# Kernel tuning notes

Hardware: AMD Instinct MI355X
Metric: run time of the kernel (lower is better)

The kernel has to match this reference:

```python
import jax, jax.numpy as jnp
import numpy as np

H = 32          # total heads
K = 8           # active heads per token
D = 128         # head_dim = embed_dim // active_heads
E = 1024        # embed_dim
S = 1024        # seq_len
MAX_SEQ = 8192
BASE = 10000.0
SCALE = D ** -0.5
LB_W = 0.01
ENT_W = 0.01


def _rope(v, cos, sin):
    # v: (T, D); cos/sin: (T, D)
    v1, v2 = v[:, : D // 2], v[:, D // 2:]
    rot = jnp.concatenate([-v2, v1], axis=-1)
    return v * cos + rot * sin


def setup_inputs() -> dict:
    key = jax.random.key(0)
    ks = jax.random.split(key, 6)
    x = jax.random.normal(ks[0], (1, S, E), jnp.float32)
    Wq = jax.random.normal(ks[1], (E, H * D), jnp.float32) * 0.02
    Wk = jax.random.normal(ks[2], (E, H * D), jnp.float32) * 0.02
    Wv = jax.random.normal(ks[3], (E, H * D), jnp.float32) * 0.02
    Wr = jax.random.normal(ks[4], (E, H), jnp.float32) * 0.02
    Wo = jax.random.normal(ks[5], (K * D, E), jnp.float32) * 0.02
    head_counts = jnp.zeros((1, H), jnp.int32)
    return {"x": x, "Wq": Wq, "Wk": Wk, "Wv": Wv, "Wr": Wr, "Wo": Wo,
            "head_counts": head_counts}


def reference(x, Wq, Wk, Wv, Wr, Wo, head_counts):
    # ---- routing (eval mode: no gumbel noise) ----
    logits = x @ Wr                                   # (1, S, H)
    soft_probs = jax.nn.softmax(logits, axis=-1)
    top_logits, head_idx = jax.lax.top_k(logits, K)   # (1, S, K)
    head_w = jax.nn.softmax(top_logits, axis=-1)      # (1, S, K)

    # ---- aux loss ----
    primary = head_idx[..., 0]                        # (1, S)
    one_hot_p = jax.nn.one_hot(primary, H, dtype=jnp.float32)
    f = one_hot_p.mean(axis=1)                        # (1, H)
    p = soft_probs.mean(axis=1)                       # (1, H)
    balance = H * (f * p).sum(axis=-1).mean()
    entropy = -(soft_probs * jnp.log(soft_probs + 1e-8)).sum(axis=-1)
    entropy_loss = -entropy.mean()
    z_loss = (jax.nn.logsumexp(logits, axis=-1) ** 2).mean() * 0.01
    aux_loss = LB_W * balance + ENT_W * entropy_loss + z_loss

    # ---- projections + per-token gather of selected heads ----
    q_all = (x @ Wq).reshape(1, S, H, D)
    k_all = (x @ Wk).reshape(1, S, H, D)
    v_all = (x @ Wv).reshape(1, S, H, D)
    gidx = head_idx[..., None]                        # (1, S, K, 1)
    q = jnp.take_along_axis(q_all, gidx, axis=2)[0].reshape(S * K, D)
    k = jnp.take_along_axis(k_all, gidx, axis=2)[0].reshape(S * K, D)
    v = jnp.take_along_axis(v_all, gidx, axis=2)[0].reshape(S * K, D)

    heads_flat = head_idx[0].reshape(S * K)           # (T,)

    # rank of each dispatched token within its head (exclusive prefix count)
    oh = jax.nn.one_hot(heads_flat, H, dtype=jnp.int32)   # (T, H)
    excl = jnp.cumsum(oh, axis=0) - oh
    rank = jnp.take_along_axis(excl, heads_flat[:, None], axis=1)[:, 0]
    positions = rank + head_counts[0, heads_flat]
    positions = jnp.clip(positions, 0, MAX_SEQ - 1)

    # ---- per-head RoPE with per-head position counters ----
    inv_freq = 1.0 / (BASE ** (jnp.arange(0, D, 2, dtype=jnp.float32) / D))
    freqs = positions.astype(jnp.float32)[:, None] * inv_freq[None, :]
    emb = jnp.concatenate([freqs, freqs], axis=-1)    # (T, D)
    cos, sin = jnp.cos(emb), jnp.sin(emb)
    q = _rope(q, cos, sin)
    k = _rope(k, cos, sin)

    # ---- block-diagonal-causal attention (same head, earlier dispatch order) ----
    idx = jnp.arange(S * K)
    mask = (heads_flat[:, None] == heads_flat[None, :]) & (idx[None, :] <= idx[:, None])
    scores = (q @ k.T) * SCALE                        # (T, T)
    scores = jnp.where(mask, scores, jnp.float32(-1e30))
    attn = jax.nn.softmax(scores, axis=-1)
    out = attn @ v                                    # (T, D)

    # ---- combine with routing weights + output projection ----
    out = out.reshape(S, K, D) * head_w[0][..., None]
    out = out.reshape(S, K * D) @ Wo                  # (S, E)
    output = out[None]                                # (1, S, E)

    updated_counts = head_counts + oh.sum(axis=0)[None]
    return output, updated_counts, aux_loss
```

## Files before the change

### kernel.cpp

```cpp
#include <hip/hip_runtime.h>
#include <math.h>

#define S 1024
#define E 1024
#define H 32
#define KSEL 8
#define D 128
#define HD 4096
#define SK 8192
#define MAXL 1024
#define CAP 9216
#define ATTN_SCALE 0.08838834764831845f
#define SSTR 36
#define PSTR 40

#define NROUTER 256
#define NCONV 832

typedef _Float16 half8 __attribute__((ext_vector_type(8)));
typedef _Float16 half4 __attribute__((ext_vector_type(4)));
typedef float floatx4 __attribute__((ext_vector_type(4)));
typedef float floatx16 __attribute__((ext_vector_type(16)));
typedef float f4 __attribute__((ext_vector_type(4)));

#define GLOAD_LDS16(gsrc, ldst) \
    __builtin_amdgcn_global_load_lds( \
        (const __attribute__((address_space(1))) void*)(gsrc), \
        (__attribute__((address_space(3))) void*)(ldst), 16, 0, 0)

__global__ __launch_bounds__(256) void router_conv_kernel(
    const float* __restrict__ x, const float* __restrict__ Wr,
    int* __restrict__ head_idx, float* __restrict__ head_w,
    float* __restrict__ pbuf, float* __restrict__ entz,
    _Float16* __restrict__ xh,
    const float* __restrict__ Wq, const float* __restrict__ Wk,
    const float* __restrict__ Wv, const float* __restrict__ Wo,
    _Float16* __restrict__ Wqkt, _Float16* __restrict__ Wot)
{
    int bid = blockIdx.x, tid = threadIdx.x;
    if (bid >= NROUTER) {
        __shared__ _Float16 tl[128 * 128];
        int cb = bid - NROUTER;
        int z, rem;
        if (cb < 768) { z = cb >> 8; rem = cb & 255; }
        else          { z = 3;       rem = cb - 768; }
        const float* W = (z == 0) ? Wq : (z == 1) ? Wk : (z == 2) ? Wv : Wo;
        _Float16* T = (z < 3) ? (Wqkt + (size_t)z * HD * E) : Wot;
        int C = (z < 3) ? HD : 1024;
        int nc = C >> 7;
        int c0 = (rem % nc) * 128;
        int r0 = (rem / nc) * 128;
        #pragma unroll
        for (int p = 0; p < 16; ++p) {
            int idx = p * 256 + tid;
            int rr = idx >> 5, cg = (idx & 31) * 4;
            f4 v = *(const f4*)&W[(size_t)(r0 + rr) * C + c0 + cg];
            half4 o;
            o.x = (_Float16)v.x; o.y = (_Float16)v.y;
            o.z = (_Float16)v.z; o.w = (_Float16)v.w;
            int sc = cg ^ (((rr >> 3) & 7) << 2);
            *(half4*)&tl[rr * 128 + sc] = o;
        }
        __syncthreads();
        #pragma unroll
        for (int p = 0; p < 8; ++p) {
            int chunk = p * 256 + tid;
            int cc = chunk >> 4, ch = chunk & 15;
            int cidx = cc ^ ((ch & 7) << 2);
            half8 o;
            #pragma unroll
            for (int j = 0; j < 8; ++j)
                o[j] = tl[(ch * 8 + j) * 128 + cidx];
            *(half8*)&T[(size_t)(c0 + cc) * 1024 + r0 + ch * 8] = o;
        }
        return;
    }
    int s = bid * 4 + (tid >> 6);
    int lane = tid & 63;
    int h = lane & 31, half = lane >> 5;
    const float* xr = x + (size_t)s * E + half * 512;
    const float* wr = Wr + (size_t)(half * 512) * H + h;
    float a0 = 0.f, a1 = 0.f, a2 = 0.f, a3 = 0.f;
    #pragma unroll 4
    for (int e = 0; e < 512; e += 4) {
        a0 += xr[e]     * wr[e * H];
        a1 += xr[e + 1] * wr[(e + 1) * H];
        a2 += xr[e + 2] * wr[(e + 2) * H];
        a3 += xr[e + 3] * wr[(e + 3) * H];
    }
    float acc = (a0 + a1) + (a2 + a3);
    acc += __shfl_xor(acc, 32, 64);
    float logit = acc;
    float m = logit;
    #pragma unroll
    for (int off = 16; off; off >>= 1) m = fmaxf(m, __shfl_xor(m, off, 64));
    float ex = expf(logit - m);
    float Z = ex;
    #pragma unroll
    for (int off = 16; off; off >>= 1) Z += __shfl_xor(Z, off, 64);
    float p = ex / Z;
    float es = p * logf(p + 1e-8f);
    #pragma unroll
    for (int off = 16; off; off >>= 1) es += __shfl_xor(es, off, 64);
    float lse = m + logf(Z);
    float lv = logit;
    float tv[KSEL]; int ti[KSEL];
    #pragma unroll
    for (int j = 0; j < KSEL; ++j) {
        float bv = lv; int bi = h;
        #pragma unroll
        for (int off = 16; off; off >>= 1) {
            float ov = __shfl_xor(bv, off, 64);
            int oi = __shfl_xor(bi, off, 64);
            if (ov > bv || (ov == bv && oi < bi)) { bv = ov; bi = oi; }
        }
        tv[j] = bv; ti[j] = bi;
        if (h == bi) lv = -INFINITY;
    }
    float Z2 = 0.f;
    #pragma unroll
    for (int j = 0; j < KSEL; ++j) Z2 += expf(tv[j] - tv[0]);
    if (lane < 32) pbuf[s * 32 + lane] = p;
    if (lane == 0) {
        entz[s * 2]     = es;
        entz[s * 2 + 1] = lse * lse;
        #pragma unroll
        for (int j = 0; j < KSEL; ++j) {
            head_idx[s * KSEL + j] = ti[j];
            head_w[s * KSEL + j]   = expf(tv[j] - tv[0]) / Z2;
        }
    }
    const float* xrow = x + (size_t)s * E;
    _Float16* xhrow = xh + (size_t)s * E;
    #pragma unroll
    for (int t = 0; t < 4; ++t) {
        int e = t * 256 + lane * 4;
        f4 v = *(const f4*)&xrow[e];
        half4 o;
        o.x = (_Float16)v.x; o.y = (_Float16)v.y; o.z = (_Float16)v.z; o.w = (_Float16)v.w;
        *(half4*)&xhrow[e] = o;
    }
}

__global__ __launch_bounds__(256) void scan_aux_kernel(
    const int* __restrict__ head_idx, const int* __restrict__ head_counts,
    int* __restrict__ order, int* __restrict__ hlen, float* __restrict__ out_counts,
    const float* __restrict__ pbuf, const float* __restrict__ entz,
    float* __restrict__ out_aux)
{
    int bid = blockIdx.x, tid = threadIdx.x;
    if (bid == H) {
        int hh = tid & 31, grp = tid >> 5;
        __shared__ float red[256], red2[256];
        __shared__ float psum[32];
        __shared__ int hist[32];
        if (tid < 32) hist[tid] = 0;
        float ps = 0.f;
        for (int s = grp; s < S; s += 8) ps += pbuf[s * 32 + hh];
        red[tid] = ps;
        float es = 0.f, zs = 0.f;
        for (int s = tid; s < S; s += 256) { es += entz[s * 2]; zs += entz[s * 2 + 1]; }
        red2[tid] = es;
        __syncthreads();
        if (grp == 0) {
            float v = 0.f;
            #pragma unroll
            for (int j = 0; j < 8; ++j) v += red[j * 32 + hh];
            psum[hh] = v;
        }
        __syncthreads();
        red[tid] = zs;
        for (int s = tid; s < S; s += 256)
            atomicAdd(&hist[head_idx[s * KSEL]], 1);
        __syncthreads();
        for (int stp = 128; stp; stp >>= 1) {
            if (tid < stp) { red[tid] += red[tid + stp]; red2[tid] += red2[tid + stp]; }
            __syncthreads();
        }
        if (tid == 0) {
            float bal = 0.f;
            for (int j = 0; j < H; ++j)
                bal += ((float)hist[j] / (float)S) * (psum[j] / (float)S);
            bal *= (float)H;
            float ent_loss = red2[0] / (float)S;
            float z = red[0] / (float)S * 0.01f;
            out_aux[0] = 0.01f * bal + 0.01f * ent_loss + z;
        }
        return;
    }
    int h = bid;
    int wave = tid >> 6, lane = tid & 63;
    __shared__ int wtot[4][4];
    int base = 0;
    int hc = head_counts[h];
    int v0 = head_idx[tid],       v1 = head_idx[256 + tid];
    int v2 = head_idx[512 + tid], v3 = head_idx[768 + tid];
    unsigned long long lt = (1ull << lane) - 1ull;
    for (int c0 = 0; c0 < SK; c0 += 1024) {
        int n0 = 0, n1 = 0, n2 = 0, n3 = 0;
        if (c0 + 1024 < SK) {
            n0 = head_idx[c0 + 1024 + tid]; n1 = head_idx[c0 + 1280 + tid];
            n2 = head_idx[c0 + 1536 + tid]; n3 = head_idx[c0 + 1792 + tid];
        }
        bool p0 = (v0 == h), p1 = (v1 == h), p2 = (v2 == h), p3 = (v3 == h);
        unsigned long long m0 = __ballot(p0), m1 = __ballot(p1);
        unsigned long long m2 = __ballot(p2), m3 = __ballot(p3);
        int w0 = __popcll(m0 & lt), w1 = __popcll(m1 & lt);
        int w2 = __popcll(m2 & lt), w3 = __popcll(m3 & lt);
        if (lane == 0) {
            wtot[0][wave] = __popcll(m0); wtot[1][wave] = __popcll(m1);
            wtot[2][wave] = __popcll(m2); wtot[3][wave] = __popcll(m3);
        }
        __syncthreads();
        int pw[4], T[4];
        #pragma unroll
        for (int i = 0; i < 4; ++i) {
            int pre = 0, tot = 0;
            #pragma unroll
            for (int w = 0; w < 4; ++w) {
                int tv = wtot[i][w];
                if (w < wave) pre += tv;
                tot += tv;
            }
            pw[i] = pre; T[i] = tot;
        }
        if (p0) order[h * MAXL + base + pw[0] + w0] = c0 + tid;
        if (p1) order[h * MAXL + base + T[0] + pw[1] + w1] = c0 + 256 + tid;
        if (p2) order[h * MAXL + base + T[0] + T[1] + pw[2] + w2] = c0 + 512 + tid;
        if (p3) order[h * MAXL + base + T[0] + T[1] + T[2] + pw[3] + w3] = c0 + 768 + tid;
        base += T[0] + T[1] + T[2] + T[3];
        __syncthreads();
        v0 = n0; v1 = n1; v2 = n2; v3 = n3;
    }
    if (tid == 0) {
        hlen[h] = base;
        out_counts[h] = (float)(hc + base);
    }
}

__global__ __launch_bounds__(256) void qkv_mfma(
    const _Float16* __restrict__ xh, const _Float16* __restrict__ Wt,
    const int* __restrict__ order, const int* __restrict__ hlen,
    const int* __restrict__ head_counts,
    _Float16* __restrict__ qh, _Float16* __restrict__ kh, _Float16* __restrict__ vT)
{
    int xid = blockIdx.x;
    int qkv = xid >> 5, h = xid & 31;
    int rt = blockIdx.y;
    int len = hlen[h];
    int row0 = rt * 64;
    if (row0 >= len) return;
    int hb = 0;
    for (int i = 0; i < h; ++i) hb += (hlen[i] + 31) & ~31;
    int lenp = (len + 31) & ~31;
    int tid = threadIdx.x, wave = tid >> 6, lane = tid & 63;
    int wm = wave >> 1, wn = wave & 1;
    int l32 = lane & 31, g = lane >> 5;

    __shared__ _Float16 Bs[2][128 * 64];

    int arow_g = row0 + wm * 32 + l32;
    int tok = (arow_g < len) ? (order[h * MAXL + arow_g] >> 3) : 0;
    const _Float16* aptr = xh + (size_t)tok * E;

    const _Float16* Wb = Wt + (size_t)((qkv * H + h) * D) * E;

    auto stageB = [&](int buf, int k0) {
        #pragma unroll
        for (int it = 0; it < 4; ++it) {
            int f = it * 256 + tid;
            int row = f >> 3, c = f & 7;
            int sc = c ^ (row & 7);
            const _Float16* src = Wb + (size_t)row * E + k0 + sc * 8;
            GLOAD_LDS16(src, &Bs[buf][f * 8]);
        }
    };

    floatx16 acc[2] = {};
    half8 a_cur[4], a_nxt[4];
    #pragma unroll
    for (int ks = 0; ks < 4; ++ks)
        a_cur[ks] = *(const half8*)(aptr + ks * 16 + g * 8);

    auto compute = [&](int buf, half8* a) {
        #pragma unroll
        for (int ks = 0; ks < 4; ++ks) {
            int wchunk = ks * 2 + g;
            #pragma unroll
            for (int nf = 0; nf < 2; ++nf) {
                int brow = wn * 64 + nf * 32 + l32;
                half8 bf = *(const half8*)&Bs[buf][brow * 64 + (wchunk ^ (brow & 7)) * 8];
                acc[nf] = __builtin_amdgcn_mfma_f32_32x32x16_f16(a[ks], bf, acc[nf], 0, 0, 0);
            }
        }
    };

    stageB(0, 0);
    __syncthreads();
    int buf = 0;
    for (int k0 = 64; k0 < E; k0 += 64) {
        stageB(buf ^ 1, k0);
        #pragma unroll
        for (int ks = 0; ks < 4; ++ks)
            a_nxt[ks] = *(const half8*)(aptr + k0 + ks * 16 + g * 8);
        compute(buf, a_cur);
        __syncthreads();
        buf ^= 1;
        #pragma unroll
        for (int ks = 0; ks < 4; ++ks) a_cur[ks] = a_nxt[ks];
    }
    compute(buf, a_cur);

    if (qkv < 2) {
        _Float16* dst = (qkv == 0) ? qh : kh;
        float* scr = (float*)&Bs[0][0];
        __syncthreads();
        #pragma unroll
        for (int nf = 0; nf < 2; ++nf) {
            int col = wn * 64 + nf * 32 + l32;
            #pragma unroll
            for (int reg = 0; reg < 16; ++reg) {
                int rl = wm * 32 + (reg & 3) + 8 * (reg >> 2) + 4 * g;
                scr[rl * 128 + col] = acc[nf][reg];
            }
        }
        __syncthreads();
        int hc = head_counts[h];
        #pragma unroll
        for (int pass = 0; pass < 16; ++pass) {
            int idx = pass * 256 + tid;
            int r = idx >> 6, d2 = idx & 63;
            int slot = row0 + r;
            if (slot < len) {
                float v1 = scr[r * 128 + d2], v2 = scr[r * 128 + 64 + d2];
                int p = slot + hc;
                p = p < 0 ? 0 : (p > 8191 ? 8191 : p);
                float inv = exp2f((float)d2 * -0.20762050f);
                float ang = (float)p * inv;
                float cs = cosf(ang), sn = sinf(ang);
                _Float16* dp = dst + ((size_t)hb + slot) * D;
                dp[d2]      = (_Float16)(v1 * cs - v2 * sn);
                dp[d2 + 64] = (_Float16)(v2 * cs + v1 * sn);
            }
        }
    } else {
        #pragma unroll
        for (int nf = 0; nf < 2; ++nf) {
            int col = wn * 64 + nf * 32 + l32;
            #pragma unroll
            for (int q4 = 0; q4 < 4; ++q4) {
                int slot0 = row0 + wm * 32 + 8 * q4 + 4 * g;
                _Float16* vp = vT + (size_t)hb * D + (size_t)col * lenp + slot0;
                if (slot0 + 3 < len) {
                    half4 o;
                    o.x = (_Float16)acc[nf][q4 * 4 + 0];
                    o.y = (_Float16)acc[nf][q4 * 4 + 1];
                    o.z = (_Float16)acc[nf][q4 * 4 + 2];
                    o.w = (_Float16)acc[nf][q4 * 4 + 3];
                    *(half4*)vp = o;
                } else {
                    #pragma unroll
                    for (int r2 = 0; r2 < 4; ++r2)
                        if (slot0 + r2 < len) vp[r2] = (_Float16)acc[nf][q4 * 4 + r2];
                }
            }
        }
    }
}

__global__ __launch_bounds__(128) void attn_mfma(
    const _Float16* __restrict__ qh, const _Float16* __restrict__ kh,
    const _Float16* __restrict__ vT,
    const int* __restrict__ order, const int* __restrict__ hlen,
    const float* __restrict__ head_w, _Float16* __restrict__ ao)
{
    int h = blockIdx.x >> 5, qt = blockIdx.x & 31;
    int len = hlen[h];
    int row0 = qt * 32;
    if (row0 >= len) return;
    int hb = 0;
    for (int i = 0; i < h; ++i) hb += (hlen[i] + 31) & ~31;
    int lenp = (len + 31) & ~31;
    int tid = threadIdx.x;
    int w = tid >> 6, lane = tid & 63;
    int l32 = lane & 31, g = lane >> 5;
    int srow = lane >> 1, shalf = lane & 1;

    __shared__ float Sld[2][32 * SSTR];
    __shared__ _Float16 Pld[2][32 * PSTR];
    __shared__ float alphaLd[2][32];
    __shared__ float mlLd[32][4];
    __shared__ float facLd[32][3];
    __shared__ int flatLd[32];
    __shared__ float Obuf[32][128];

    if (tid < 32) {
        int r = row0 + tid;
        flatLd[tid] = (r < len) ? order[h * MAXL + r] : -1;
    }

    const _Float16* qrow = qh + ((size_t)hb + row0 + l32) * D;
    half8 qf[8];
    #pragma unroll
    for (int t = 0; t < 8; ++t) qf[t] = *(const half8*)(qrow + t * 16 + g * 8);

    floatx16 O[4] = {};
    float m_run = -INFINITY, l_run = 0.f;

    if (w <= qt) {
        half8 kf[8], kfn[8], vv[8];
        {
            const _Float16* krow = kh + ((size_t)hb + w * 32 + l32) * D;
            #pragma unroll
            for (int t = 0; t < 8; ++t) kf[t] = *(const half8*)(krow + t * 16 + g * 8);
        }
        for (int kt = w; kt <= qt; kt += 2) {
            int col0 = kt * 32;
            floatx16 Sc = {};
            #pragma unroll
            for (int t = 0; t < 8; ++t)
                Sc = __builtin_amdgcn_mfma_f32_32x32x16_f16(qf[t], kf[t], Sc, 0, 0, 0);
            #pragma unroll
            for (int nt = 0; nt < 4; ++nt) {
                const _Float16* vp = vT + (size_t)hb * D + (size_t)(nt * 32 + l32) * lenp + col0;
                vv[nt * 2]     = *(const half8*)(vp + g * 8);
                vv[nt * 2 + 1] = *(const half8*)(vp + 16 + g * 8);
            }
            if (kt + 2 <= qt) {
                const _Float16* krow = kh + ((size_t)hb + col0 + 64 + l32) * D;
                #pragma unroll
                for (int t = 0; t < 8; ++t) kfn[t] = *(const half8*)(krow + t * 16 + g * 8);
            }
            bool diag = (kt == qt);
            #pragma unroll
            for (int reg = 0; reg < 16; ++reg) {
                int row = (reg & 3) + 8 * (reg >> 2) + 4 * g;
                float s = Sc[reg] * ATTN_SCALE;
                if (diag && l32 > row) s = -1e30f;
                Sld[w][row * SSTR + l32] = s;
            }
            __builtin_amdgcn_wave_barrier();
            const float* sp = &Sld[w][srow * SSTR + shalf * 16];
            float va[16];
            *(f4*)(va)      = *(const f4*)(sp);
            *(f4*)(va + 4)  = *(const f4*)(sp + 4);
            *(f4*)(va + 8)  = *(const f4*)(sp + 8);
            *(f4*)(va + 12) = *(const f4*)(sp + 12);
            float mt_ = va[0];
            #pragma unroll
            for (int j = 1; j < 16; ++j) mt_ = fmaxf(mt_, va[j]);
            mt_ = fmaxf(mt_, __shfl_xor(mt_, 1, 64));
            float m_new = fmaxf(m_run, mt_);
            float alpha = __expf(m_run - m_new);
            float p[16], tsum = 0.f;
            #pragma unroll
            for (int j = 0; j < 16; ++j) { p[j] = __expf(va[j] - m_new); tsum += p[j]; }
            tsum += __shfl_xor(tsum, 1, 64);
            l_run = l_run * alpha + tsum;
            m_run = m_new;
            half8 ph0, ph1;
            #pragma unroll
            for (int j = 0; j < 8; ++j) { ph0[j] = (_Float16)p[j]; ph1[j] = (_Float16)p[j + 8]; }
            *(half8*)&Pld[w][srow * PSTR + shalf * 16]     = ph0;
            *(half8*)&Pld[w][srow * PSTR + shalf * 16 + 8] = ph1;
            if (shalf == 0) alphaLd[w][srow] = alpha;
            __builtin_amdgcn_wave_barrier();
            f4 al[4];
            #pragma unroll
            for (int qq = 0; qq < 4; ++qq) al[qq] = *(const f4*)&alphaLd[w][4 * g + 8 * qq];
            #pragma unroll
            for (int reg = 0; reg < 16; ++reg) {
                float av = al[reg >> 2][reg & 3];
                O[0][reg] *= av; O[1][reg] *= av; O[2][reg] *= av; O[3][reg] *= av;
            }
            half8 pf0 = *(const half8*)&Pld[w][l32 * PSTR + g * 8];
            half8 pf1 = *(const half8*)&Pld[w][l32 * PSTR + 16 + g * 8];
            #pragma unroll
            for (int nt = 0; nt < 4; ++nt) {
                O[nt] = __builtin_amdgcn_mfma_f32_32x32x16_f16(pf0, vv[nt * 2],     O[nt], 0, 0, 0);
                O[nt] = __builtin_amdgcn_mfma_f32_32x32x16_f16(pf1, vv[nt * 2 + 1], O[nt], 0, 0, 0);
            }
            __builtin_amdgcn_wave_barrier();
            #pragma unroll
            for (int t = 0; t < 8; ++t) kf[t] = kfn[t];
        }
    }
    if (shalf == 0) { mlLd[srow][w * 2] = m_run; mlLd[srow][w * 2 + 1] = l_run; }
    __syncthreads();
    if (tid < 32) {
        float m0 = mlLd[tid][0], l0 = mlLd[tid][1];
        float m1 = mlLd[tid][2], l1 = mlLd[tid][3];
        float ms = fmaxf(m0, m1);
        float f0 = __expf(m0 - ms), f1 = __expf(m1 - ms);
        float lt = f0 * l0 + f1 * l1;
        int flat = flatLd[tid];
        float hw = (flat >= 0) ? head_w[flat] : 0.f;
        facLd[tid][0] = f1;
        facLd[tid][1] = hw / lt;
        facLd[tid][2] = f0;
    }
    __syncthreads();
    if (w == 1) {
        #pragma unroll
        for (int nt = 0; nt < 4; ++nt) {
            int col = nt * 32 + l32;
            #pragma unroll
            for (int reg = 0; reg < 16; ++reg) {
                int row = (reg & 3) + 8 * (reg >> 2) + 4 * g;
                Obuf[row][col] = O[nt][reg] * facLd[row][0];
            }
        }
    }
    __syncthreads();
    if (w == 0) {
        #pragma unroll
        for (int nt = 0; nt < 4; ++nt) {
            int col = nt * 32 + l32;
            #pragma unroll
            for (int reg = 0; reg < 16; ++reg) {
                int row = (reg & 3) + 8 * (reg >> 2) + 4 * g;
                int flat = flatLd[row];
                if (flat >= 0) {
                    float val = (O[nt][reg] * facLd[row][2] + Obuf[row][col]) * facLd[row][1];
                    ao[(size_t)flat * D + col] = (_Float16)val;
                }
            }
        }
    }
}

__global__ __launch_bounds__(256) void out_mfma(
    const _Float16* __restrict__ A, const _Float16* __restrict__ Bt,
    float* __restrict__ C)
{
    int n0 = blockIdx.x * 64, m0 = blockIdx.y * 64;
    int tid = threadIdx.x, wave = tid >> 6, lane = tid & 63;
    int wm = wave >> 1, wn = wave & 1;
    int l32 = lane & 31, g = lane >> 5;

    __shared__ _Float16 Bs[2][64 * 64];

    const _Float16* aptr = A + (size_t)(m0 + wm * 32 + l32) * 1024;

    auto stageB = [&](int buf, int k0) {
        #pragma unroll
        for (int it = 0; it < 2; ++it) {
            int f = it * 256 + tid;
            int row = f >> 3, c = f & 7;
            int sc = c ^ (row & 7);
            GLOAD_LDS16(Bt + (size_t)(n0 + row) * 1024 + k0 + sc * 8, &Bs[buf][f * 8]);
        }
    };

    floatx16 acc = {};
    int brow = wn * 32 + l32;
    half8 a_cur[4], a_nxt[4];
    #pragma unroll
    for (int ks = 0; ks < 4; ++ks)
        a_cur[ks] = *(const half8*)(aptr + ks * 16 + g * 8);

    auto compute = [&](int buf, half8* a) {
        #pragma unroll
        for (int ks = 0; ks < 4; ++ks) {
            int wchunk = ks * 2 + g;
            half8 bf = *(const half8*)&Bs[buf][brow * 64 + (wchunk ^ (brow & 7)) * 8];
            acc = __builtin_amdgcn_mfma_f32_32x32x16_f16(a[ks], bf, acc, 0, 0, 0);
        }
    };

    stageB(0, 0);
    __syncthreads();
    int buf = 0;
    for (int k0 = 64; k0 < 1024; k0 += 64) {
        stageB(buf ^ 1, k0);
        #pragma unroll
        for (int ks = 0; ks < 4; ++ks)
            a_nxt[ks] = *(const half8*)(aptr + k0 + ks * 16 + g * 8);
        compute(buf, a_cur);
        __syncthreads();
        buf ^= 1;
        #pragma unroll
        for (int ks = 0; ks < 4; ++ks) a_cur[ks] = a_nxt[ks];
    }
    compute(buf, a_cur);

    int col = n0 + wn * 32 + l32;
    #pragma unroll
    for (int reg = 0; reg < 16; ++reg) {
        int row = m0 + wm * 32 + (reg & 3) + 8 * (reg >> 2) + 4 * g;
        C[(size_t)row * 1024 + col] = acc[reg];
    }
}

extern "C" void kernel_launch(void* const* d_in, const int* in_sizes, int n_in,
                              void* d_out, int out_size, void* d_ws, size_t ws_size,
                              hipStream_t stream)
{
    const float* x  = (const float*)d_in[0];
    const float* Wq = (const float*)d_in[1];
    const float* Wk = (const float*)d_in[2];
    const float* Wv = (const float*)d_in[3];
    const float* Wr = (const float*)d_in[4];
    const float* Wo = (const float*)d_in[5];
    const int* head_counts = (const int*)d_in[6];
    float* out = (float*)d_out;

    float* head_w = (float*)d_ws;
    float* pbuf   = head_w + SK;
    float* entz   = pbuf + S * 32;
    int* head_idx = (int*)(entz + S * 2);
    int* order    = head_idx + SK;
    int* hlen     = order + H * MAXL;
    _Float16* xh   = (_Float16*)(hlen + 64);
    _Float16* aoh  = xh + (size_t)S * E;
    _Float16* Wqkt = aoh + (size_t)SK * D;
    _Float16* Wot  = Wqkt + (size_t)3 * HD * E;
    _Float16* qh   = Wot + (size_t)1024 * 1024;
    _Float16* kh   = qh + (size_t)CAP * D;
    _Float16* vT   = kh + (size_t)CAP * D;

    router_conv_kernel<<<NROUTER + NCONV, 256, 0, stream>>>(
        x, Wr, head_idx, head_w, pbuf, entz, xh, Wq, Wk, Wv, Wo, Wqkt, Wot);
    scan_aux_kernel<<<33, 256, 0, stream>>>(head_idx, head_counts, order, hlen,
                                            out + (size_t)S * E, pbuf, entz,
                                            out + (size_t)S * E + H);
    qkv_mfma<<<dim3(96, 16), 256, 0, stream>>>(xh, Wqkt, order, hlen, head_counts,
                                               qh, kh, vT);
    attn_mfma<<<H * 32, 128, 0, stream>>>(qh, kh, vT, order, hlen, head_w, aoh);
    out_mfma<<<dim3(16, 16), 256, 0, stream>>>(aoh, Wot, out);
}
```

Before: 222.4 us.

## Precompute RoPE cos/sin table and compute head offsets with wave prefix scan

Adds a table of cos/sin values for every position and frequency (8192x64 float2), built by extra blocks in the router kernel, and moves weight conversion into its own kernel launch. The QKV epilogue reads cos/sin from this table instead of calling exp2f/cosf/sinf per element. The serial per-thread loop over hlen that computed each head's base offset is replaced by a wave-level shuffle prefix scan. It also zero-fills the padded V slots. The cost is a 4 MB table write and read, plus one more kernel launch.

Measured after the change: 226.8 us. 2.0% more time.

```diff
diff --git a/kernel.cpp b/kernel.cpp
--- a/kernel.cpp
+++ b/kernel.cpp
@@ -15,11 +15,10 @@
 #define PSTR 40
 
 #define NROUTER 256
-#define NCONV 832
+#define NTAB 512
 
 typedef _Float16 half8 __attribute__((ext_vector_type(8)));
 typedef _Float16 half4 __attribute__((ext_vector_type(4)));
-typedef float floatx4 __attribute__((ext_vector_type(4)));
 typedef float floatx16 __attribute__((ext_vector_type(16)));
 typedef float f4 __attribute__((ext_vector_type(4)));
 
@@ -28,50 +27,82 @@
         (const __attribute__((address_space(1))) void*)(gsrc), \
         (__attribute__((address_space(3))) void*)(ldst), 16, 0, 0)
 
-__global__ __launch_bounds__(256) void router_conv_kernel(
+__device__ __forceinline__ void head_prefix(const int* __restrict__ hlen, int h,
+                                            int lane, int& len, int& hb, int& lenp)
+{
+    int hl = (lane < 32) ? hlen[lane] : 0;
+    int hp = (hl + 31) & ~31;
+    int pref = hp;
+    #pragma unroll
+    for (int off = 1; off < 32; off <<= 1) {
+        int t = __shfl_up(pref, off, 64);
+        if (lane >= off) pref += t;
+    }
+    int excl = pref - hp;
+    hb   = __shfl(excl, h, 64);
+    len  = __shfl(hl, h, 64);
+    lenp = (len + 31) & ~31;
+}
+
+__global__ __launch_bounds__(256) void conv_kernel(
+    const float* __restrict__ Wq, const float* __restrict__ Wk,
+    const float* __restrict__ Wv, const float* __restrict__ Wo,
+    _Float16* __restrict__ Wqkt, _Float16* __restrict__ Wot)
+{
+    int cb = blockIdx.x, tid = threadIdx.x;
+    __shared__ _Float16 tl[128 * 128];
+    int z, rem;
+    if (cb < 768) { z = cb >> 8; rem = cb & 255; }
+    else          { z = 3;       rem = cb - 768; }
+    const float* W = (z == 0) ? Wq : (z == 1) ? Wk : (z == 2) ? Wv : Wo;
+    _Float16* T = (z < 3) ? (Wqkt + (size_t)z * HD * E) : Wot;
+    int C = (z < 3) ? HD : 1024;
+    int nc = C >> 7;
+    int c0 = (rem % nc) * 128;
+    int r0 = (rem / nc) * 128;
+    #pragma unroll
+    for (int p = 0; p < 16; ++p) {
+        int idx = p * 256 + tid;
+        int rr = idx >> 5, cg = (idx & 31) * 4;
+        f4 v = *(const f4*)&W[(size_t)(r0 + rr) * C + c0 + cg];
+        half4 o;
+        o.x = (_Float16)v.x; o.y = (_Float16)v.y;
+        o.z = (_Float16)v.z; o.w = (_Float16)v.w;
+        int sc = cg ^ (((rr >> 3) & 7) << 2);
+        *(half4*)&tl[rr * 128 + sc] = o;
+    }
+    __syncthreads();
+    #pragma unroll
+    for (int p = 0; p < 8; ++p) {
+        int chunk = p * 256 + tid;
+        int cc = chunk >> 4, ch = chunk & 15;
+        int cidx = cc ^ ((ch & 7) << 2);
+        half8 o;
+        #pragma unroll
+        for (int j = 0; j < 8; ++j)
+            o[j] = tl[(ch * 8 + j) * 128 + cidx];
+        *(half8*)&T[(size_t)(c0 + cc) * 1024 + r0 + ch * 8] = o;
+    }
+}
+
+__global__ __launch_bounds__(256) void router_tab_kernel(
     const float* __restrict__ x, const float* __restrict__ Wr,
     int* __restrict__ head_idx, float* __restrict__ head_w,
     float* __restrict__ pbuf, float* __restrict__ entz,
-    _Float16* __restrict__ xh,
-    const float* __restrict__ Wq, const float* __restrict__ Wk,
-    const float* __restrict__ Wv, const float* __restrict__ Wo,
-    _Float16* __restrict__ Wqkt, _Float16* __restrict__ Wot)
+    _Float16* __restrict__ xh, float2* __restrict__ tab)
 {
     int bid = blockIdx.x, tid = threadIdx.x;
     if (bid >= NROUTER) {
-        __shared__ _Float16 tl[128 * 128];
-        int cb = bid - NROUTER;
-        int z, rem;
-        if (cb < 768) { z = cb >> 8; rem = cb & 255; }
-        else          { z = 3;       rem = cb - 768; }
-        const float* W = (z == 0) ? Wq : (z == 1) ? Wk : (z == 2) ? Wv : Wo;
-        _Float16* T = (z < 3) ? (Wqkt + (size_t)z * HD * E) : Wot;
-        int C = (z < 3) ? HD : 1024;
-        int nc = C >> 7;
-        int c0 = (rem % nc) * 128;
-        int r0 = (rem / nc) * 128;
-        #pragma unroll
-        for (int p = 0; p < 16; ++p) {
-            int idx = p * 256 + tid;
-            int rr = idx >> 5, cg = (idx & 31) * 4;
-            f4 v = *(const f4*)&W[(size_t)(r0 + rr) * C + c0 + cg];
-            half4 o;
-            o.x = (_Float16)v.x; o.y = (_Float16)v.y;
-            o.z = (_Float16)v.z; o.w = (_Float16)v.w;
-            int sc = cg ^ (((rr >> 3) & 7) << 2);
-            *(half4*)&tl[rr * 128 + sc] = o;
-        }
-        __syncthreads();
-        #pragma unroll
-        for (int p = 0; p < 8; ++p) {
-            int chunk = p * 256 + tid;
-            int cc = chunk >> 4, ch = chunk & 15;
-            int cidx = cc ^ ((ch & 7) << 2);
-            half8 o;
-            #pragma unroll
-            for (int j = 0; j < 8; ++j)
-                o[j] = tl[(ch * 8 + j) * 128 + cidx];
-            *(half8*)&T[(size_t)(c0 + cc) * 1024 + r0 + ch * 8] = o;
+        int base = (bid - NROUTER) * 1024;
+        #pragma unroll
+        for (int j = 0; j < 4; ++j) {
+            int idx = base + j * 256 + tid;
+            int p = idx >> 6, d2 = idx & 63;
+            float inv = exp2f((float)d2 * -0.20762050f);
+            float ang = (float)p * inv;
+            float sn, cs;
+            sincosf(ang, &sn, &cs);
+            tab[idx] = make_float2(cs, sn);
         }
         return;
     }
@@ -241,19 +272,17 @@
 __global__ __launch_bounds__(256) void qkv_mfma(
     const _Float16* __restrict__ xh, const _Float16* __restrict__ Wt,
     const int* __restrict__ order, const int* __restrict__ hlen,
-    const int* __restrict__ head_counts,
+    const int* __restrict__ head_counts, const float2* __restrict__ tab,
     _Float16* __restrict__ qh, _Float16* __restrict__ kh, _Float16* __restrict__ vT)
 {
     int xid = blockIdx.x;
     int qkv = xid >> 5, h = xid & 31;
     int rt = blockIdx.y;
-    int len = hlen[h];
+    int tid = threadIdx.x, wave = tid >> 6, lane = tid & 63;
+    int len, hb, lenp;
+    head_prefix(hlen, h, lane, len, hb, lenp);
     int row0 = rt * 64;
     if (row0 >= len) return;
-    int hb = 0;
-    for (int i = 0; i < h; ++i) hb += (hlen[i] + 31) & ~31;
-    int lenp = (len + 31) & ~31;
-    int tid = threadIdx.x, wave = tid >> 6, lane = tid & 63;
     int wm = wave >> 1, wn = wave & 1;
     int l32 = lane & 31, g = lane >> 5;
 
@@ -262,7 +291,6 @@
     int arow_g = row0 + wm * 32 + l32;
     int tok = (arow_g < len) ? (order[h * MAXL + arow_g] >> 3) : 0;
     const _Float16* aptr = xh + (size_t)tok * E;
-
     const _Float16* Wb = Wt + (size_t)((qkv * H + h) * D) * E;
 
     auto stageB = [&](int buf, int k0) {
@@ -335,12 +363,10 @@
                 float v1 = scr[r * 128 + d2], v2 = scr[r * 128 + 64 + d2];
                 int p = slot + hc;
                 p = p < 0 ? 0 : (p > 8191 ? 8191 : p);
-                float inv = exp2f((float)d2 * -0.20762050f);
-                float ang = (float)p * inv;
-                float cs = cosf(ang), sn = sinf(ang);
+                float2 tt = tab[p * 64 + d2];
                 _Float16* dp = dst + ((size_t)hb + slot) * D;
-                dp[d2]      = (_Float16)(v1 * cs - v2 * sn);
-                dp[d2 + 64] = (_Float16)(v2 * cs + v1 * sn);
+                dp[d2]      = (_Float16)(v1 * tt.x - v2 * tt.y);
+                dp[d2 + 64] = (_Float16)(v2 * tt.x + v1 * tt.y);
             }
         }
     } else {
@@ -360,8 +386,11 @@
                     *(half4*)vp = o;
                 } else {
                     #pragma unroll
-                    for (int r2 = 0; r2 < 4; ++r2)
-                        if (slot0 + r2 < len) vp[r2] = (_Float16)acc[nf][q4 * 4 + r2];
+                    for (int r2 = 0; r2 < 4; ++r2) {
+                        int sl = slot0 + r2;
+                        if (sl < len) vp[r2] = (_Float16)acc[nf][q4 * 4 + r2];
+                        else if (sl < lenp) vp[r2] = (_Float16)0.f;
+                    }
                 }
             }
         }
@@ -375,14 +404,12 @@
     const float* __restrict__ head_w, _Float16* __restrict__ ao)
 {
     int h = blockIdx.x >> 5, qt = blockIdx.x & 31;
-    int len = hlen[h];
+    int tid = threadIdx.x;
+    int w = tid >> 6, lane = tid & 63;
+    int len, hb, lenp;
+    head_prefix(hlen, h, lane, len, hb, lenp);
     int row0 = qt * 32;
     if (row0 >= len) return;
-    int hb = 0;
-    for (int i = 0; i < h; ++i) hb += (hlen[i] + 31) & ~31;
-    int lenp = (len + 31) & ~31;
-    int tid = threadIdx.x;
-    int w = tid >> 6, lane = tid & 63;
     int l32 = lane & 31, g = lane >> 5;
     int srow = lane >> 1, shalf = lane & 1;
 
@@ -618,13 +645,15 @@
     _Float16* qh   = Wot + (size_t)1024 * 1024;
     _Float16* kh   = qh + (size_t)CAP * D;
     _Float16* vT   = kh + (size_t)CAP * D;
-
-    router_conv_kernel<<<NROUTER + NCONV, 256, 0, stream>>>(
-        x, Wr, head_idx, head_w, pbuf, entz, xh, Wq, Wk, Wv, Wo, Wqkt, Wot);
+    float2* tab    = (float2*)(vT + (size_t)CAP * D);
+
+    router_tab_kernel<<<NROUTER + NTAB, 256, 0, stream>>>(
+        x, Wr, head_idx, head_w, pbuf, entz, xh, tab);
+    conv_kernel<<<832, 256, 0, stream>>>(Wq, Wk, Wv, Wo, Wqkt, Wot);
     scan_aux_kernel<<<33, 256, 0, stream>>>(head_idx, head_counts, order, hlen,
                                             out + (size_t)S * E, pbuf, entz,
                                             out + (size_t)S * E + H);
-    qkv_mfma<<<dim3(96, 16), 256, 0, stream>>>(xh, Wqkt, order, hlen, head_counts,
+    qkv_mfma<<<dim3(96, 16), 256, 0, stream>>>(xh, Wqkt, order, hlen, head_counts, tab,
                                                qh, kh, vT);
     attn_mfma<<<H * 32, 128, 0, stream>>>(qh, kh, vT, order, hlen, head_w, aoh);
     out_mfma<<<dim3(16, 16), 256, 0, stream>>>(aoh, Wot, out);
```
